# Optimization experiments

Measured on AMD Instinct MI355X. Metric: run time of the kernel, lower is better.

The kernel has to match this reference:

```python
import jax, jax.numpy as jnp
import numpy as np

B, NOBJ, MLEN, D, H = 32, 256, 256, 1024, 16
DK = D // H
NEG = -1e9


def setup_inputs() -> dict:
    key = jax.random.key(0)
    ks = jax.random.split(key, 16)

    def lin(kw, kb, fin, fout):
        s = 1.0 / np.sqrt(fin)
        w = jax.random.uniform(kw, (fin, fout), jnp.float32, -s, s)
        b = jax.random.uniform(kb, (fout,), jnp.float32, -s, s)
        return w, b

    v = jax.random.normal(ks[0], (B, NOBJ, D), jnp.float32)
    q = jax.random.normal(ks[1], (B, MLEN, D), jnp.float32)
    v_mask = jax.random.randint(ks[2], (B, NOBJ), 0, 2).astype(jnp.float32)
    q_mask = jax.random.randint(ks[3], (B, MLEN), 0, 2).astype(jnp.float32)
    # guarantee at least one valid position per row (avoid 0/0 in masked mean)
    v_mask = v_mask.at[:, 0].set(1.0)
    q_mask = q_mask.at[:, 0].set(1.0)

    w_v4q, b_v4q = lin(ks[4], ks[5], D, D)
    w_q4v, b_q4v = lin(ks[6], ks[7], D, D)
    w_vlin, b_vlin = lin(ks[8], ks[9], D, 3 * D)
    w_qlin, b_qlin = lin(ks[10], ks[11], D, 3 * D)
    w_vout, b_vout = lin(ks[12], ks[13], D, D)
    w_qout, b_qout = lin(ks[14], ks[15], D, D)

    return dict(v=v, q=q, v_mask=v_mask, q_mask=q_mask,
                w_v4q=w_v4q, b_v4q=b_v4q, w_q4v=w_q4v, b_q4v=b_q4v,
                w_vlin=w_vlin, b_vlin=b_vlin, w_qlin=w_qlin, b_qlin=b_qlin,
                w_vout=w_vout, b_vout=b_vout, w_qout=w_qout, b_qout=b_qout)


def _attend(qh, kh, vh, mask):
    # qh,kh,vh: [B,N,D]; mask: [B,N]
    b, n, _ = qh.shape
    qh = qh.reshape(b, n, H, DK)
    kh = kh.reshape(b, n, H, DK)
    vh = vh.reshape(b, n, H, DK)
    scores = jnp.einsum('bqhd,bkhd->bhqk', qh, kh)
    # faithful to torch: masked_fill(-1e9) THEN divide by sqrt(dk)
    scores = jnp.where(mask[:, None, None, :] == 0, NEG, scores) / np.sqrt(DK)
    attn = jax.nn.softmax(scores, axis=-1)
    out = jnp.einsum('bhqk,bkhd->bqhd', attn, vh)
    return out.reshape(b, n, H * DK)


def reference(v, q, v_mask, q_mask,
              w_v4q, b_v4q, w_q4v, b_q4v,
              w_vlin, b_vlin, w_qlin, b_qlin,
              w_vout, b_vout, w_qout, b_qout):
    v_mean = (v * v_mask[:, :, None]).sum(1) / v_mask.sum(1, keepdims=True)
    q_mean = (q * q_mask[:, :, None]).sum(1) / q_mask.sum(1, keepdims=True)
    v4q_gate = jax.nn.sigmoid(jax.nn.relu(v_mean) @ w_v4q + b_v4q)[:, None, :]
    q4v_gate = jax.nn.sigmoid(jax.nn.relu(q_mean) @ w_q4v + b_q4v)[:, None, :]

    v_trans = (jax.nn.relu(v) @ w_vlin + b_vlin) * v_mask[:, :, None]
    q_trans = (jax.nn.relu(q) @ w_qlin + b_qlin) * q_mask[:, :, None]
    v_k, v_q, v_v = jnp.split(v_trans, 3, axis=2)
    q_k, q_q, q_v = jnp.split(q_trans, 3, axis=2)

    v_update = _attend((1 + q4v_gate) * v_q, (1 + q4v_gate) * v_k, v_v, v_mask)
    q_update = _attend((1 + v4q_gate) * q_q, (1 + v4q_gate) * q_k, q_v, q_mask)

    updated_v = (v + v_update) @ w_vout + b_vout
    updated_q = (q + q_update) @ w_qout + b_qout
    return updated_v, updated_q
```

## Files before the change

kernel.cpp:

```cpp
#include <hip/hip_runtime.h>
#include <cstdint>

typedef unsigned short u16;
typedef __attribute__((ext_vector_type(8))) short s16x8;
typedef __attribute__((ext_vector_type(4))) float f32x4;

__device__ __forceinline__ u16 f2bf(float f) {
  unsigned int u = __float_as_uint(f);
  unsigned int r = u + 0x7FFFu + ((u >> 16) & 1u);
  return (u16)(r >> 16);
}
__device__ __forceinline__ float bf2f(u16 b) {
  return __uint_as_float(((unsigned int)b) << 16);
}
__device__ __forceinline__ f32x4 mfma16(s16x8 a, s16x8 b, f32x4 c) {
  return __builtin_amdgcn_mfma_f32_16x16x32_bf16(a, b, c, 0, 0, 0);
}
__device__ __forceinline__ void gload16(const void* g, void* l) {
  __builtin_amdgcn_global_load_lds((const __attribute__((address_space(1))) void*)g,
                                   (__attribute__((address_space(3))) void*)l, 16, 0, 0);
}

__global__ __launch_bounds__(256) void k_transpose_cast(const float* __restrict__ in,
                                                        u16* __restrict__ out,
                                                        int K, int N) {
  __shared__ float tile[32][33];
  int n0 = blockIdx.x * 32, k0 = blockIdx.y * 32;
  int tx = threadIdx.x & 31, ty = threadIdx.x >> 5;
#pragma unroll
  for (int i = 0; i < 32; i += 8)
    tile[ty + i][tx] = in[(size_t)(k0 + ty + i) * N + n0 + tx];
  __syncthreads();
#pragma unroll
  for (int i = 0; i < 32; i += 8)
    out[(size_t)(n0 + ty + i) * K + k0 + tx] = f2bf(tile[tx][ty + i]);
}

__global__ __launch_bounds__(256) void k_mean(const float* __restrict__ v,
                                              const float* __restrict__ q,
                                              const float* __restrict__ vm,
                                              const float* __restrict__ qm,
                                              float* __restrict__ rmean_v,
                                              float* __restrict__ rmean_q) {
  int b = blockIdx.x, dc = blockIdx.y, mod = blockIdx.z;
  const float* x  = mod ? q : v;
  const float* mk = mod ? qm : vm;
  float* out      = mod ? rmean_q : rmean_v;
  int d = dc * 256 + threadIdx.x;
  const float* xb = x + (size_t)b * 256 * 1024 + d;
  const float* mb = mk + b * 256;
  float s = 0.f, ms = 0.f;
  for (int n = 0; n < 256; ++n) {
    float m = mb[n];
    ms += m;
    s = fmaf(xb[(size_t)n * 1024], m, s);
  }
  float mean = s / ms;
  out[b * 1024 + d] = mean > 0.f ? mean : 0.f;
}

__global__ __launch_bounds__(256) void k_gate(const float* __restrict__ rmean,
                                              const float* __restrict__ W,
                                              const float* __restrict__ bias,
                                              float* __restrict__ gs) {
  int b = blockIdx.y;
  int d = blockIdx.x * 256 + threadIdx.x;
  const float* r = rmean + b * 1024;
  float acc = bias[d];
#pragma unroll 8
  for (int k = 0; k < 1024; ++k) acc = fmaf(r[k], W[(size_t)k * 1024 + d], acc);
  gs[b * 1024 + d] = 1.f + 1.f / (1.f + expf(-acc));
}

__global__ __launch_bounds__(256) void k_relucast(const float* __restrict__ v,
                                                  const float* __restrict__ q,
                                                  u16* __restrict__ ov,
                                                  u16* __restrict__ oq) {
  const float* x = blockIdx.z ? q : v;
  u16* o = blockIdx.z ? oq : ov;
  size_t i = (size_t)blockIdx.x * 256 + threadIdx.x;
  const f32x4* xv = (const f32x4*)x;
  f32x4 a = xv[2 * i], b = xv[2 * i + 1];
  s16x8 r;
#pragma unroll
  for (int j = 0; j < 4; ++j) r[j] = (short)f2bf(a[j] > 0.f ? a[j] : 0.f);
#pragma unroll
  for (int j = 0; j < 4; ++j) r[4 + j] = (short)f2bf(b[j] > 0.f ? b[j] : 0.f);
  ((s16x8*)o)[i] = r;
}

template <int EPI>
__global__ __launch_bounds__(512, 2) void k_mm(const u16* __restrict__ A,
                                               const u16* __restrict__ BTv,
                                               const u16* __restrict__ BTq,
                                               const float* __restrict__ biasv,
                                               const float* __restrict__ biasq,
                                               u16* __restrict__ outv_b,
                                               u16* __restrict__ outq_b,
                                               float* __restrict__ outf,
                                               const float* __restrict__ maskv,
                                               const float* __restrict__ maskq,
                                               const float* __restrict__ gsv,
                                               const float* __restrict__ gsq,
                                               int NBX) {
  __shared__ u16 lA[3][8192];
  __shared__ u16 lB[3][16384];
  int nwg = gridDim.x;
  int cpx = nwg >> 3;
  int bid = blockIdx.x;
  int id = (bid & 7) * cpx + (bid >> 3);
  int bx = id % NBX, by = id / NBX;
  int m0 = by * 128, n0 = bx * 256;
  int half = (m0 >= 8192);
  const u16* BT = half ? BTq : BTv;
  const float* bias = half ? biasq : biasv;

  int tid = threadIdx.x;
  int w = tid >> 6, lane = tid & 63;
  int wr = w >> 2, wc = w & 3;
  int la = lane & 15, lb = lane >> 4;

  const char* srcA[2]; const char* srcB[4];
  int dstAo[2], dstBo[4];
#pragma unroll
  for (int i = 0; i < 2; ++i) {
    int o = i * 8192 + tid * 16;
    int row = o >> 7, colb = o & 127;
    srcA[i] = (const char*)(A + (size_t)(m0 + row) * 1024) + (colb ^ ((row & 7) << 4));
    dstAo[i] = o;
  }
#pragma unroll
  for (int i = 0; i < 4; ++i) {
    int o = i * 8192 + tid * 16;
    int row = o >> 7, colb = o & 127;
    srcB[i] = (const char*)(BT + (size_t)(n0 + row) * 1024) + (colb ^ ((row & 7) << 4));
    dstBo[i] = o;
  }
  auto stageA = [&](int tt, int i) {
    gload16(srcA[i] + tt * 128, (char*)&lA[tt % 3][0] + dstAo[i]);
  };
  auto stageB = [&](int tt, int i) {
    gload16(srcB[i] + tt * 128, (char*)&lB[tt % 3][0] + dstBo[i]);
  };
  auto rdA = [&](int buf, int i, int h) {
    int row = wr * 64 + i * 16 + la;
    int cb = (h * 64 + lb * 16) ^ ((row & 7) << 4);
    return *(const s16x8*)((const char*)&lA[buf][0] + row * 128 + cb);
  };
  auto rdB = [&](int buf, int j, int h) {
    int row = wc * 64 + j * 16 + la;
    int cb = (h * 64 + lb * 16) ^ ((row & 7) << 4);
    return *(const s16x8*)((const char*)&lB[buf][0] + row * 128 + cb);
  };

  f32x4 acc[4][4] = {};

#pragma unroll
  for (int i = 0; i < 2; ++i) stageA(0, i);
#pragma unroll
  for (int i = 0; i < 4; ++i) stageB(0, i);
#pragma unroll
  for (int i = 0; i < 2; ++i) stageA(1, i);
#pragma unroll
  for (int i = 0; i < 4; ++i) stageB(1, i);
  asm volatile("s_waitcnt vmcnt(6)" ::: "memory");
  __builtin_amdgcn_s_barrier();

  for (int t = 0; t < 16; ++t) {
    int buf = t % 3;
    bool pf = (t + 2 < 16);
    s16x8 af[4], bf_[4];
#pragma unroll
    for (int i = 0; i < 4; ++i) af[i] = rdA(buf, i, 0);
#pragma unroll
    for (int j = 0; j < 4; ++j) bf_[j] = rdB(buf, j, 0);
    if (pf) { stageA(t + 2, 0); stageA(t + 2, 1); stageB(t + 2, 0); }
    __builtin_amdgcn_s_barrier();
    asm volatile("s_waitcnt lgkmcnt(0)" ::: "memory");
    __builtin_amdgcn_sched_barrier(0);
    __builtin_amdgcn_s_setprio(1);
#pragma unroll
    for (int i = 0; i < 4; ++i)
#pragma unroll
      for (int j = 0; j < 4; ++j)
        acc[i][j] = mfma16(af[i], bf_[j], acc[i][j]);
    __builtin_amdgcn_s_setprio(0);
    __builtin_amdgcn_s_barrier();
#pragma unroll
    for (int i = 0; i < 4; ++i) af[i] = rdA(buf, i, 1);
#pragma unroll
    for (int j = 0; j < 4; ++j) bf_[j] = rdB(buf, j, 1);
    if (pf) { stageB(t + 2, 1); stageB(t + 2, 2); stageB(t + 2, 3); }
    __builtin_amdgcn_s_barrier();
    asm volatile("s_waitcnt lgkmcnt(0)" ::: "memory");
    __builtin_amdgcn_sched_barrier(0);
    __builtin_amdgcn_s_setprio(1);
#pragma unroll
    for (int i = 0; i < 4; ++i)
#pragma unroll
      for (int j = 0; j < 4; ++j)
        acc[i][j] = mfma16(af[i], bf_[j], acc[i][j]);
    __builtin_amdgcn_s_setprio(0);
    if (pf) asm volatile("s_waitcnt vmcnt(6)" ::: "memory");
    else    asm volatile("s_waitcnt vmcnt(0)" ::: "memory");
    __builtin_amdgcn_s_barrier();
  }

  u16* outb = half ? outq_b : outv_b;
  const float* mask = half ? maskq : maskv;
  const float* gs = half ? gsq : gsv;
#pragma unroll
  for (int i = 0; i < 4; ++i) {
    int mbase = m0 + wr * 64 + i * 16 + lb * 4;
#pragma unroll
    for (int j = 0; j < 4; ++j) {
      int n = n0 + wc * 64 + j * 16 + la;
      float bn = bias[n];
#pragma unroll
      for (int r = 0; r < 4; ++r) {
        int m = mbase + r;
        float val = acc[i][j][r] + bn;
        if (EPI == 0) {
          int mloc = m & 8191;
          val *= mask[mloc];
          if (n < 2048) val *= gs[((mloc >> 8) << 10) + (n & 1023)];
          outb[(size_t)mloc * 3072 + n] = f2bf(val);
        } else {
          outf[(size_t)m * 1024 + n] = val;
        }
      }
    }
  }
}

__global__ __launch_bounds__(256) void k_attn(const u16* __restrict__ trans,
                                              const float* __restrict__ mask,
                                              const float* __restrict__ xorig,
                                              u16* __restrict__ attin) {
  __shared__ u16 Kl[16384];
  __shared__ u16 Vt[64 * 256];
  int h = blockIdx.x >> 2, qc = blockIdx.x & 3;
  int b = blockIdx.y;
  int t = threadIdx.x, w = t >> 6, lane = t & 63;
  const u16* tb = trans + (size_t)b * 256 * 3072;
  const char* tbc = (const char*)tb;

#pragma unroll
  for (int i = 0; i < 8; ++i) {
    int o = i * 4096 + t * 16;
    int row = o >> 7, colb = o & 127;
    gload16(tbc + (size_t)row * 6144 + h * 128 + (colb ^ ((row & 7) << 4)),
            (char*)Kl + o);
  }
#pragma unroll
  for (int i = 0; i < 8; ++i) {
    int c = t + i * 256;
    int key = c >> 3, dc = c & 7;
    s16x8 vv = *(const s16x8*)(tb + (size_t)key * 3072 + 2048 + h * 64 + dc * 8);
    int quad = key >> 3, klow = key & 7;
#pragma unroll
    for (int j = 0; j < 8; ++j) {
      int d = dc * 8 + j;
      Vt[d * 256 + ((quad ^ (d & 7)) << 3) + klow] = (u16)vv[j];
    }
  }
  __syncthreads();

  int la = lane & 15, lb = lane >> 4;
  int q0 = qc * 64 + w * 16;
  const u16* qrow = tb + (size_t)(q0 + la) * 3072 + 1024 + h * 64;
  s16x8 qf0 = *(const s16x8*)(qrow + lb * 8);
  s16x8 qf1 = *(const s16x8*)(qrow + 32 + lb * 8);

  f32x4 sc[16];
#pragma unroll
  for (int nt = 0; nt < 16; ++nt) {
    int row = nt * 16 + la;
    int sw = (row & 7) << 4;
    s16x8 kf0 = *(const s16x8*)((const char*)Kl + row * 128 + ((lb * 16) ^ sw));
    s16x8 kf1 = *(const s16x8*)((const char*)Kl + row * 128 + ((64 + lb * 16) ^ sw));
    f32x4 s = {0.f, 0.f, 0.f, 0.f};
    s = mfma16(qf0, kf0, s);
    s = mfma16(qf1, kf1, s);
    sc[nt] = s;
  }
  __syncthreads();

  u16* Pw = Kl + w * 4096;
  const float* mb = mask + b * 256;
  float rsum[4] = {0.f, 0.f, 0.f, 0.f};
#pragma unroll
  for (int nt = 0; nt < 16; ++nt) {
    int key = nt * 16 + la;
    float km = mb[key];
    int quad = key >> 3, klow = key & 7;
#pragma unroll
    for (int r = 0; r < 4; ++r) {
      float p = (km != 0.f) ? expf(sc[nt][r] * 0.125f) : 0.f;
      u16 pb = f2bf(p);
      int lr = lb * 4 + r;
      rsum[r] += bf2f(pb);
      Pw[lr * 256 + ((quad ^ (lr & 7)) << 3) + klow] = pb;
    }
  }
#pragma unroll
  for (int r = 0; r < 4; ++r) {
    rsum[r] += __shfl_xor(rsum[r], 1);
    rsum[r] += __shfl_xor(rsum[r], 2);
    rsum[r] += __shfl_xor(rsum[r], 4);
    rsum[r] += __shfl_xor(rsum[r], 8);
  }

  f32x4 o[4] = {};
  for (int kt = 0; kt < 8; ++kt) {
    int pq = kt * 4 + lb;
    s16x8 pa = *(const s16x8*)&Pw[la * 256 + ((pq ^ (la & 7)) << 3)];
#pragma unroll
    for (int dt = 0; dt < 4; ++dt) {
      int d = dt * 16 + la;
      s16x8 vb = *(const s16x8*)&Vt[d * 256 + ((pq ^ (d & 7)) << 3)];
      o[dt] = mfma16(pa, vb, o[dt]);
    }
  }

#pragma unroll
  for (int dt = 0; dt < 4; ++dt) {
    int dcol = h * 64 + dt * 16 + la;
#pragma unroll
    for (int r = 0; r < 4; ++r) {
      int qr = q0 + lb * 4 + r;
      size_t gi = ((size_t)b * 256 + qr) * 1024 + dcol;
      attin[gi] = f2bf(xorig[gi] + o[dt][r] / rsum[r]);
    }
  }
}

extern "C" void kernel_launch(void* const* d_in, const int* in_sizes, int n_in,
                              void* d_out, int out_size, void* d_ws, size_t ws_size,
                              hipStream_t stream) {
  const float* v      = (const float*)d_in[0];
  const float* q      = (const float*)d_in[1];
  const float* v_mask = (const float*)d_in[2];
  const float* q_mask = (const float*)d_in[3];
  const float* w_v4q  = (const float*)d_in[4];
  const float* b_v4q  = (const float*)d_in[5];
  const float* w_q4v  = (const float*)d_in[6];
  const float* b_q4v  = (const float*)d_in[7];
  const float* w_vlin = (const float*)d_in[8];
  const float* b_vlin = (const float*)d_in[9];
  const float* w_qlin = (const float*)d_in[10];
  const float* b_qlin = (const float*)d_in[11];
  const float* w_vout = (const float*)d_in[12];
  const float* b_vout = (const float*)d_in[13];
  const float* w_qout = (const float*)d_in[14];
  const float* b_qout = (const float*)d_in[15];
  float* out = (float*)d_out;

  char* ws = (char*)d_ws;
  u16* rbf_v     = (u16*)(ws);
  u16* rbf_q     = (u16*)(ws + 16777216);
  u16* trans_v   = (u16*)(ws + 33554432);
  u16* wlinT_v   = (u16*)(ws + 83886080);
  u16* wlinT_q   = (u16*)(ws + 90177536);
  u16* woutT_v   = (u16*)(ws + 96468992);
  u16* woutT_q   = (u16*)(ws + 98566144);
  float* rmean_v = (float*)(ws + 100663296);
  float* rmean_q = (float*)(ws + 100794368);
  float* gs_v    = (float*)(ws + 100925440);
  float* gs_q    = (float*)(ws + 101056512);
  u16* trans_q   = (u16*)d_out;

  dim3 blk(256);
  k_transpose_cast<<<dim3(96, 32), blk, 0, stream>>>(w_vlin, wlinT_v, 1024, 3072);
  k_transpose_cast<<<dim3(96, 32), blk, 0, stream>>>(w_qlin, wlinT_q, 1024, 3072);
  k_transpose_cast<<<dim3(32, 32), blk, 0, stream>>>(w_vout, woutT_v, 1024, 1024);
  k_transpose_cast<<<dim3(32, 32), blk, 0, stream>>>(w_qout, woutT_q, 1024, 1024);
  k_mean<<<dim3(32, 4, 2), blk, 0, stream>>>(v, q, v_mask, q_mask, rmean_v, rmean_q);
  k_gate<<<dim3(4, 32), blk, 0, stream>>>(rmean_q, w_q4v, b_q4v, gs_v);
  k_gate<<<dim3(4, 32), blk, 0, stream>>>(rmean_v, w_v4q, b_v4q, gs_q);
  k_relucast<<<dim3(4096, 1, 2), blk, 0, stream>>>(v, q, rbf_v, rbf_q);
  k_mm<0><<<dim3(1536), dim3(512), 0, stream>>>(rbf_v, wlinT_v, wlinT_q,
                                                b_vlin, b_qlin, trans_v, trans_q,
                                                nullptr, v_mask, q_mask, gs_v, gs_q, 12);
  k_attn<<<dim3(64, 32), blk, 0, stream>>>(trans_v, v_mask, v, rbf_v);
  k_attn<<<dim3(64, 32), blk, 0, stream>>>(trans_q, q_mask, q, rbf_q);
  k_mm<1><<<dim3(512), dim3(512), 0, stream>>>(rbf_v, woutT_v, woutT_q,
                                               b_vout, b_qout, nullptr, nullptr,
                                               out, nullptr, nullptr, nullptr, nullptr, 4);
}
```

Baseline: 625.7 us.

## Fuse prep kernels, enlarge GEMM tiles, pre-transpose V, merge attention launches

Fuses the masked-mean and relu-cast passes into one kernel that reduces partial sums with atomics, and folds the relu and divide into the gate kernel. The GEMM switches to 256x256 tiles with a 32-wide K step and a 4-deep LDS ring. A separate kernel now pre-transposes the V slices so attention can load them with async global-to-LDS copies instead of scalar scatter. Paired launches for the weight transposes, gates and both attention modalities are merged via blockIdx.z. This cuts launch count and the redundant input reads, at the cost of atomics, a memset and an extra V transpose pass.

```diff
diff --git a/kernel.cpp b/kernel.cpp
--- a/kernel.cpp
+++ b/kernel.cpp
@@ -7,8 +7,7 @@
 
 __device__ __forceinline__ u16 f2bf(float f) {
   unsigned int u = __float_as_uint(f);
-  unsigned int r = u + 0x7FFFu + ((u >> 16) & 1u);
-  return (u16)(r >> 16);
+  return (u16)((u + 0x7FFFu + ((u >> 16) & 1u)) >> 16);
 }
 __device__ __forceinline__ float bf2f(u16 b) {
   return __uint_as_float(((unsigned int)b) << 16);
@@ -21,9 +20,11 @@
                                    (__attribute__((address_space(3))) void*)l, 16, 0, 0);
 }
 
-__global__ __launch_bounds__(256) void k_transpose_cast(const float* __restrict__ in,
-                                                        u16* __restrict__ out,
-                                                        int K, int N) {
+__global__ __launch_bounds__(256) void k_wt(const float* __restrict__ in0, u16* __restrict__ out0,
+                                            const float* __restrict__ in1, u16* __restrict__ out1,
+                                            int K, int N) {
+  const float* in = blockIdx.z ? in1 : in0;
+  u16* out = blockIdx.z ? out1 : out0;
   __shared__ float tile[32][33];
   int n0 = blockIdx.x * 32, k0 = blockIdx.y * 32;
   int tx = threadIdx.x & 31, ty = threadIdx.x >> 5;
@@ -36,57 +37,60 @@
     out[(size_t)(n0 + ty + i) * K + k0 + tx] = f2bf(tile[tx][ty + i]);
 }
 
-__global__ __launch_bounds__(256) void k_mean(const float* __restrict__ v,
+__global__ __launch_bounds__(256) void k_prep(const float* __restrict__ v,
                                               const float* __restrict__ q,
                                               const float* __restrict__ vm,
                                               const float* __restrict__ qm,
-                                              float* __restrict__ rmean_v,
-                                              float* __restrict__ rmean_q) {
-  int b = blockIdx.x, dc = blockIdx.y, mod = blockIdx.z;
-  const float* x  = mod ? q : v;
-  const float* mk = mod ? qm : vm;
-  float* out      = mod ? rmean_q : rmean_v;
+                                              u16* __restrict__ rbf,
+                                              float* __restrict__ raw,
+                                              float* __restrict__ msum) {
+  int b = blockIdx.x;
+  int mod = blockIdx.y & 1, dc = blockIdx.y >> 1;
+  int ns = blockIdx.z;
+  const float* x = mod ? q : v;
+  const float* mk = (mod ? qm : vm) + b * 256;
   int d = dc * 256 + threadIdx.x;
-  const float* xb = x + (size_t)b * 256 * 1024 + d;
-  const float* mb = mk + b * 256;
-  float s = 0.f, ms = 0.f;
-  for (int n = 0; n < 256; ++n) {
-    float m = mb[n];
-    ms += m;
-    s = fmaf(xb[(size_t)n * 1024], m, s);
-  }
-  float mean = s / ms;
-  out[b * 1024 + d] = mean > 0.f ? mean : 0.f;
-}
-
-__global__ __launch_bounds__(256) void k_gate(const float* __restrict__ rmean,
-                                              const float* __restrict__ W,
-                                              const float* __restrict__ bias,
-                                              float* __restrict__ gs) {
-  int b = blockIdx.y;
+  const float* xb = x + ((size_t)b * 256 + ns * 32) * 1024 + d;
+  u16* ob = rbf + ((size_t)(mod * 8192 + b * 256 + ns * 32)) * 1024 + d;
+  float s = 0.f;
+#pragma unroll 4
+  for (int n = 0; n < 32; ++n) {
+    float xv = xb[(size_t)n * 1024];
+    s = fmaf(xv, mk[ns * 32 + n], s);
+    ob[(size_t)n * 1024] = f2bf(xv > 0.f ? xv : 0.f);
+  }
+  atomicAdd(&raw[(mod * 32 + b) * 1024 + d], s);
+  if (threadIdx.x == 0 && dc == 0) {
+    float t = 0.f;
+    for (int n = 0; n < 32; ++n) t += mk[ns * 32 + n];
+    atomicAdd(&msum[mod * 32 + b], t);
+  }
+}
+
+__global__ __launch_bounds__(256) void k_gate(const float* __restrict__ raw,
+                                              const float* __restrict__ msum,
+                                              const float* __restrict__ Wq4v,
+                                              const float* __restrict__ bq4v,
+                                              const float* __restrict__ Wv4q,
+                                              const float* __restrict__ bv4q,
+                                              float* __restrict__ gsv,
+                                              float* __restrict__ gsq) {
+  int b = blockIdx.y, z = blockIdx.z;
+  int srcmod = z == 0 ? 1 : 0;
+  const float* W = z == 0 ? Wq4v : Wv4q;
+  const float* bias = z == 0 ? bq4v : bv4q;
+  float* gs = z == 0 ? gsv : gsq;
+  const float* r = raw + (srcmod * 32 + b) * 1024;
+  float inv = 1.f / msum[srcmod * 32 + b];
   int d = blockIdx.x * 256 + threadIdx.x;
-  const float* r = rmean + b * 1024;
   float acc = bias[d];
 #pragma unroll 8
-  for (int k = 0; k < 1024; ++k) acc = fmaf(r[k], W[(size_t)k * 1024 + d], acc);
+  for (int k = 0; k < 1024; ++k) {
+    float m = r[k] * inv;
+    m = m > 0.f ? m : 0.f;
+    acc = fmaf(m, W[(size_t)k * 1024 + d], acc);
+  }
   gs[b * 1024 + d] = 1.f + 1.f / (1.f + expf(-acc));
-}
-
-__global__ __launch_bounds__(256) void k_relucast(const float* __restrict__ v,
-                                                  const float* __restrict__ q,
-                                                  u16* __restrict__ ov,
-                                                  u16* __restrict__ oq) {
-  const float* x = blockIdx.z ? q : v;
-  u16* o = blockIdx.z ? oq : ov;
-  size_t i = (size_t)blockIdx.x * 256 + threadIdx.x;
-  const f32x4* xv = (const f32x4*)x;
-  f32x4 a = xv[2 * i], b = xv[2 * i + 1];
-  s16x8 r;
-#pragma unroll
-  for (int j = 0; j < 4; ++j) r[j] = (short)f2bf(a[j] > 0.f ? a[j] : 0.f);
-#pragma unroll
-  for (int j = 0; j < 4; ++j) r[4 + j] = (short)f2bf(b[j] > 0.f ? b[j] : 0.f);
-  ((s16x8*)o)[i] = r;
 }
 
 template <int EPI>
@@ -101,80 +105,72 @@
                                                const float* __restrict__ maskv,
                                                const float* __restrict__ maskq,
                                                const float* __restrict__ gsv,
-                                               const float* __restrict__ gsq,
-                                               int NBX) {
-  __shared__ u16 lA[3][8192];
-  __shared__ u16 lB[3][16384];
-  int nwg = gridDim.x;
-  int cpx = nwg >> 3;
-  int bid = blockIdx.x;
+                                               const float* __restrict__ gsq) {
+  __shared__ u16 lA[4][8192];
+  __shared__ u16 lB[4][8192];
+  constexpr int NU = 32;
+  int nwg = gridDim.x, cpx = nwg >> 3, bid = blockIdx.x;
   int id = (bid & 7) * cpx + (bid >> 3);
-  int bx = id % NBX, by = id / NBX;
-  int m0 = by * 128, n0 = bx * 256;
+  int by = id & 63, bx = id >> 6;
+  int m0 = by * 256, n0 = bx * 256;
   int half = (m0 >= 8192);
   const u16* BT = half ? BTq : BTv;
-  const float* bias = half ? biasq : biasv;
-
-  int tid = threadIdx.x;
-  int w = tid >> 6, lane = tid & 63;
+
+  int tid = threadIdx.x, w = tid >> 6, lane = tid & 63;
   int wr = w >> 2, wc = w & 3;
   int la = lane & 15, lb = lane >> 4;
 
-  const char* srcA[2]; const char* srcB[4];
-  int dstAo[2], dstBo[4];
-#pragma unroll
-  for (int i = 0; i < 2; ++i) {
-    int o = i * 8192 + tid * 16;
-    int row = o >> 7, colb = o & 127;
-    srcA[i] = (const char*)(A + (size_t)(m0 + row) * 1024) + (colb ^ ((row & 7) << 4));
-    dstAo[i] = o;
-  }
-#pragma unroll
-  for (int i = 0; i < 4; ++i) {
-    int o = i * 8192 + tid * 16;
-    int row = o >> 7, colb = o & 127;
-    srcB[i] = (const char*)(BT + (size_t)(n0 + row) * 1024) + (colb ^ ((row & 7) << 4));
-    dstBo[i] = o;
-  }
-  auto stageA = [&](int tt, int i) {
-    gload16(srcA[i] + tt * 128, (char*)&lA[tt % 3][0] + dstAo[i]);
-  };
-  auto stageB = [&](int tt, int i) {
-    gload16(srcB[i] + tt * 128, (char*)&lB[tt % 3][0] + dstBo[i]);
-  };
-  auto rdA = [&](int buf, int i, int h) {
-    int row = wr * 64 + i * 16 + la;
-    int cb = (h * 64 + lb * 16) ^ ((row & 7) << 4);
-    return *(const s16x8*)((const char*)&lA[buf][0] + row * 128 + cb);
-  };
-  auto rdB = [&](int buf, int j, int h) {
-    int row = wc * 64 + j * 16 + la;
-    int cb = (h * 64 + lb * 16) ^ ((row & 7) << 4);
-    return *(const s16x8*)((const char*)&lB[buf][0] + row * 128 + cb);
-  };
-
-  f32x4 acc[4][4] = {};
-
-#pragma unroll
-  for (int i = 0; i < 2; ++i) stageA(0, i);
-#pragma unroll
-  for (int i = 0; i < 4; ++i) stageB(0, i);
-#pragma unroll
-  for (int i = 0; i < 2; ++i) stageA(1, i);
-#pragma unroll
-  for (int i = 0; i < 4; ++i) stageB(1, i);
-  asm volatile("s_waitcnt vmcnt(6)" ::: "memory");
+  const char* srcA[2]; const char* srcB[2]; int dstO[2];
+#pragma unroll
+  for (int s = 0; s < 2; ++s) {
+    int o = s * 8192 + tid * 16;
+    int row = o >> 6, colb = o & 63;
+    int sw = (row & 3) << 4;
+    srcA[s] = (const char*)A + (size_t)(m0 + row) * 2048 + (colb ^ sw);
+    srcB[s] = (const char*)BT + (size_t)(n0 + row) * 2048 + (colb ^ sw);
+    dstO[s] = o;
+  }
+  int aoffs[8], boffs[4];
+#pragma unroll
+  for (int i = 0; i < 8; ++i) {
+    int r = wr * 128 + i * 16 + la;
+    aoffs[i] = r * 64 + ((lb * 16) ^ ((r & 3) << 4));
+  }
+#pragma unroll
+  for (int j = 0; j < 4; ++j) {
+    int r = wc * 64 + j * 16 + la;
+    boffs[j] = r * 64 + ((lb * 16) ^ ((r & 3) << 4));
+  }
+
+  f32x4 acc[8][4] = {};
+
+#pragma unroll
+  for (int s = 0; s < 2; ++s) gload16(srcA[s], (char*)&lA[0][0] + dstO[s]);
+#pragma unroll
+  for (int s = 0; s < 2; ++s) gload16(srcB[s], (char*)&lB[0][0] + dstO[s]);
+#pragma unroll
+  for (int s = 0; s < 2; ++s) gload16(srcA[s] + 64, (char*)&lA[1][0] + dstO[s]);
+#pragma unroll
+  for (int s = 0; s < 2; ++s) gload16(srcB[s] + 64, (char*)&lB[1][0] + dstO[s]);
+  asm volatile("s_waitcnt vmcnt(4)" ::: "memory");
   __builtin_amdgcn_s_barrier();
 
-  for (int t = 0; t < 16; ++t) {
-    int buf = t % 3;
-    bool pf = (t + 2 < 16);
-    s16x8 af[4], bf_[4];
-#pragma unroll
-    for (int i = 0; i < 4; ++i) af[i] = rdA(buf, i, 0);
-#pragma unroll
-    for (int j = 0; j < 4; ++j) bf_[j] = rdB(buf, j, 0);
-    if (pf) { stageA(t + 2, 0); stageA(t + 2, 1); stageB(t + 2, 0); }
+  for (int u = 0; u < NU; ++u) {
+    const char* cA = (const char*)&lA[u & 3][0];
+    const char* cB = (const char*)&lB[u & 3][0];
+    int pu = u + 2;
+    char* wA = (char*)&lA[pu & 3][0];
+    char* wB = (char*)&lB[pu & 3][0];
+    bool pf = pu < NU;
+    s16x8 a0[4], b0[4];
+#pragma unroll
+    for (int j = 0; j < 4; ++j) b0[j] = *(const s16x8*)(cB + boffs[j]);
+#pragma unroll
+    for (int i = 0; i < 4; ++i) a0[i] = *(const s16x8*)(cA + aoffs[i]);
+    if (pf) {
+      gload16(srcA[0] + pu * 64, wA + dstO[0]);
+      gload16(srcA[1] + pu * 64, wA + dstO[1]);
+    }
     __builtin_amdgcn_s_barrier();
     asm volatile("s_waitcnt lgkmcnt(0)" ::: "memory");
     __builtin_amdgcn_sched_barrier(0);
@@ -183,14 +179,16 @@
     for (int i = 0; i < 4; ++i)
 #pragma unroll
       for (int j = 0; j < 4; ++j)
-        acc[i][j] = mfma16(af[i], bf_[j], acc[i][j]);
+        acc[i][j] = mfma16(a0[i], b0[j], acc[i][j]);
     __builtin_amdgcn_s_setprio(0);
     __builtin_amdgcn_s_barrier();
-#pragma unroll
-    for (int i = 0; i < 4; ++i) af[i] = rdA(buf, i, 1);
-#pragma unroll
-    for (int j = 0; j < 4; ++j) bf_[j] = rdB(buf, j, 1);
-    if (pf) { stageB(t + 2, 1); stageB(t + 2, 2); stageB(t + 2, 3); }
+    s16x8 a1[4];
+#pragma unroll
+    for (int i = 0; i < 4; ++i) a1[i] = *(const s16x8*)(cA + aoffs[4 + i]);
+    if (pf) {
+      gload16(srcB[0] + pu * 64, wB + dstO[0]);
+      gload16(srcB[1] + pu * 64, wB + dstO[1]);
+    }
     __builtin_amdgcn_s_barrier();
     asm volatile("s_waitcnt lgkmcnt(0)" ::: "memory");
     __builtin_amdgcn_sched_barrier(0);
@@ -199,19 +197,19 @@
     for (int i = 0; i < 4; ++i)
 #pragma unroll
       for (int j = 0; j < 4; ++j)
-        acc[i][j] = mfma16(af[i], bf_[j], acc[i][j]);
+        acc[4 + i][j] = mfma16(a1[i], b0[j], acc[4 + i][j]);
     __builtin_amdgcn_s_setprio(0);
-    if (pf) asm volatile("s_waitcnt vmcnt(6)" ::: "memory");
-    else    asm volatile("s_waitcnt vmcnt(0)" ::: "memory");
+    if (u < NU - 2) asm volatile("s_waitcnt vmcnt(4)" ::: "memory");
+    else            asm volatile("s_waitcnt vmcnt(0)" ::: "memory");
     __builtin_amdgcn_s_barrier();
   }
 
-  u16* outb = half ? outq_b : outv_b;
+  const float* bias = half ? biasq : biasv;
   const float* mask = half ? maskq : maskv;
   const float* gs = half ? gsq : gsv;
 #pragma unroll
-  for (int i = 0; i < 4; ++i) {
-    int mbase = m0 + wr * 64 + i * 16 + lb * 4;
+  for (int i = 0; i < 8; ++i) {
+    int mbase = m0 + wr * 128 + i * 16 + lb * 4;
 #pragma unroll
     for (int j = 0; j < 4; ++j) {
       int n = n0 + wc * 64 + j * 16 + la;
@@ -224,7 +222,7 @@
           int mloc = m & 8191;
           val *= mask[mloc];
           if (n < 2048) val *= gs[((mloc >> 8) << 10) + (n & 1023)];
-          outb[(size_t)mloc * 3072 + n] = f2bf(val);
+          (half ? outq_b : outv_b)[(size_t)mloc * 3072 + n] = f2bf(val);
         } else {
           outf[(size_t)m * 1024 + n] = val;
         }
@@ -233,10 +231,56 @@
   }
 }
 
-__global__ __launch_bounds__(256) void k_attn(const u16* __restrict__ trans,
-                                              const float* __restrict__ mask,
-                                              const float* __restrict__ xorig,
-                                              u16* __restrict__ attin) {
+__global__ __launch_bounds__(256) void k_vtrans(const u16* __restrict__ tr0,
+                                                const u16* __restrict__ tr1,
+                                                u16* __restrict__ vt0,
+                                                u16* __restrict__ vt1) {
+  int bz = blockIdx.z;
+  int mod = bz >> 5, b = bz & 31;
+  const u16* tr = mod ? tr1 : tr0;
+  u16* vt = mod ? vt1 : vt0;
+  __shared__ u16 tile[64 * 64];
+  int kt = blockIdx.x, dt = blockIdx.y;
+  int t = threadIdx.x, tx = t & 7, ty = t >> 3;
+  const u16* src = tr + (size_t)b * 786432 + 2048 + dt * 64;
+#pragma unroll
+  for (int i = 0; i < 2; ++i) {
+    int key = ty + i * 32;
+    s16x8 vv = *(const s16x8*)(src + (size_t)(kt * 64 + key) * 3072 + tx * 8);
+    int oct = key >> 3;
+#pragma unroll
+    for (int j = 0; j < 8; ++j) {
+      int d = tx * 8 + j;
+      tile[d * 64 + ((oct ^ (d >> 3)) << 3) + (key & 7)] = (u16)vv[j];
+    }
+  }
+  __syncthreads();
+  u16* dst = vt + (size_t)b * 262144 + (size_t)dt * 64 * 256 + kt * 64;
+#pragma unroll
+  for (int i = 0; i < 2; ++i) {
+    int d = ty + i * 32;
+    s16x8 ov = *(const s16x8*)&tile[d * 64 + ((tx ^ (d >> 3)) << 3)];
+    *(s16x8*)(dst + (size_t)d * 256 + tx * 8) = ov;
+  }
+}
+
+__global__ __launch_bounds__(256) void k_attn(const u16* __restrict__ tr0,
+                                              const u16* __restrict__ tr1,
+                                              const u16* __restrict__ vt0,
+                                              const u16* __restrict__ vt1,
+                                              const float* __restrict__ mk0,
+                                              const float* __restrict__ mk1,
+                                              const float* __restrict__ x0,
+                                              const float* __restrict__ x1,
+                                              u16* __restrict__ ao0,
+                                              u16* __restrict__ ao1) {
+  int z = blockIdx.z;
+  const u16* trans = z ? tr1 : tr0;
+  const u16* vt = z ? vt1 : vt0;
+  const float* mask = z ? mk1 : mk0;
+  const float* xorig = z ? x1 : x0;
+  u16* attin = z ? ao1 : ao0;
+
   __shared__ u16 Kl[16384];
   __shared__ u16 Vt[64 * 256];
   int h = blockIdx.x >> 2, qc = blockIdx.x & 3;
@@ -252,17 +296,12 @@
     gload16(tbc + (size_t)row * 6144 + h * 128 + (colb ^ ((row & 7) << 4)),
             (char*)Kl + o);
   }
+  const char* vtb = (const char*)(vt + (size_t)b * 262144 + (size_t)h * 64 * 256);
 #pragma unroll
   for (int i = 0; i < 8; ++i) {
-    int c = t + i * 256;
-    int key = c >> 3, dc = c & 7;
-    s16x8 vv = *(const s16x8*)(tb + (size_t)key * 3072 + 2048 + h * 64 + dc * 8);
-    int quad = key >> 3, klow = key & 7;
-#pragma unroll
-    for (int j = 0; j < 8; ++j) {
-      int d = dc * 8 + j;
-      Vt[d * 256 + ((quad ^ (d & 7)) << 3) + klow] = (u16)vv[j];
-    }
+    int o = i * 4096 + t * 16;
+    int d = o >> 9, oct = (o >> 4) & 31;
+    gload16(vtb + d * 512 + ((oct ^ (d & 7)) << 4), (char*)Vt + o);
   }
   __syncthreads();
 
@@ -310,6 +349,7 @@
     rsum[r] += __shfl_xor(rsum[r], 4);
     rsum[r] += __shfl_xor(rsum[r], 8);
   }
+  __syncthreads();
 
   f32x4 o[4] = {};
   for (int kt = 0; kt < 8; ++kt) {
@@ -357,34 +397,35 @@
   float* out = (float*)d_out;
 
   char* ws = (char*)d_ws;
-  u16* rbf_v     = (u16*)(ws);
+  u16* rbf       = (u16*)(ws);
+  u16* rbf_v     = rbf;
   u16* rbf_q     = (u16*)(ws + 16777216);
-  u16* trans_v   = (u16*)(ws + 33554432);
-  u16* wlinT_v   = (u16*)(ws + 83886080);
-  u16* wlinT_q   = (u16*)(ws + 90177536);
-  u16* woutT_v   = (u16*)(ws + 96468992);
-  u16* woutT_q   = (u16*)(ws + 98566144);
-  float* rmean_v = (float*)(ws + 100663296);
-  float* rmean_q = (float*)(ws + 100794368);
-  float* gs_v    = (float*)(ws + 100925440);
-  float* gs_q    = (float*)(ws + 101056512);
+  u16* woutT_v   = (u16*)(ws + 33554432);
+  u16* woutT_q   = (u16*)(ws + 35651584);
+  u16* trans_v   = (u16*)(ws + 37748736);
+  u16* wlinT_v   = (u16*)(ws + 88080384);
+  u16* wlinT_q   = (u16*)(ws + 94371840);
+  float* raw     = (float*)(ws + 100663296);
+  float* msum    = (float*)(ws + 100925440);
+  float* gs_v    = (float*)(ws + 100925696);
+  float* gs_q    = (float*)(ws + 101056768);
+  u16* vT_v      = (u16*)(ws + 88080384);
   u16* trans_q   = (u16*)d_out;
+  u16* vT_q      = (u16*)((char*)d_out + 50331648);
 
   dim3 blk(256);
-  k_transpose_cast<<<dim3(96, 32), blk, 0, stream>>>(w_vlin, wlinT_v, 1024, 3072);
-  k_transpose_cast<<<dim3(96, 32), blk, 0, stream>>>(w_qlin, wlinT_q, 1024, 3072);
-  k_transpose_cast<<<dim3(32, 32), blk, 0, stream>>>(w_vout, woutT_v, 1024, 1024);
-  k_transpose_cast<<<dim3(32, 32), blk, 0, stream>>>(w_qout, woutT_q, 1024, 1024);
-  k_mean<<<dim3(32, 4, 2), blk, 0, stream>>>(v, q, v_mask, q_mask, rmean_v, rmean_q);
-  k_gate<<<dim3(4, 32), blk, 0, stream>>>(rmean_q, w_q4v, b_q4v, gs_v);
-  k_gate<<<dim3(4, 32), blk, 0, stream>>>(rmean_v, w_v4q, b_v4q, gs_q);
-  k_relucast<<<dim3(4096, 1, 2), blk, 0, stream>>>(v, q, rbf_v, rbf_q);
-  k_mm<0><<<dim3(1536), dim3(512), 0, stream>>>(rbf_v, wlinT_v, wlinT_q,
-                                                b_vlin, b_qlin, trans_v, trans_q,
-                                                nullptr, v_mask, q_mask, gs_v, gs_q, 12);
-  k_attn<<<dim3(64, 32), blk, 0, stream>>>(trans_v, v_mask, v, rbf_v);
-  k_attn<<<dim3(64, 32), blk, 0, stream>>>(trans_q, q_mask, q, rbf_q);
-  k_mm<1><<<dim3(512), dim3(512), 0, stream>>>(rbf_v, woutT_v, woutT_q,
-                                               b_vout, b_qout, nullptr, nullptr,
-                                               out, nullptr, nullptr, nullptr, nullptr, 4);
-}
+  hipMemsetAsync(raw, 0, 262400, stream);
+  k_wt<<<dim3(96, 32, 2), blk, 0, stream>>>(w_vlin, wlinT_v, w_qlin, wlinT_q, 1024, 3072);
+  k_wt<<<dim3(32, 32, 2), blk, 0, stream>>>(w_vout, woutT_v, w_qout, woutT_q, 1024, 1024);
+  k_prep<<<dim3(32, 8, 8), blk, 0, stream>>>(v, q, v_mask, q_mask, rbf, raw, msum);
+  k_gate<<<dim3(4, 32, 2), blk, 0, stream>>>(raw, msum, w_q4v, b_q4v, w_v4q, b_v4q, gs_v, gs_q);
+  k_mm<0><<<dim3(768), dim3(512), 0, stream>>>(rbf, wlinT_v, wlinT_q, b_vlin, b_qlin,
+                                               trans_v, trans_q, nullptr,
+                                               v_mask, q_mask, gs_v, gs_q);
+  k_vtrans<<<dim3(4, 16, 64), blk, 0, stream>>>(trans_v, trans_q, vT_v, vT_q);
+  k_attn<<<dim3(64, 32, 2), blk, 0, stream>>>(trans_v, trans_q, vT_v, vT_q,
+                                              v_mask, q_mask, v, q, rbf_v, rbf_q);
+  k_mm<1><<<dim3(256), dim3(512), 0, stream>>>(rbf, woutT_v, woutT_q, b_vout, b_qout,
+                                               nullptr, nullptr, out,
+                                               nullptr, nullptr, nullptr, nullptr);
+}
```

Result: faster. 546.3 us (-12.7%).
